# Performance work log

Measured on AMD Instinct MI355X. Metric: run time of the kernel, lower is better.

## Reference

```python
import jax, jax.numpy as jnp
import numpy as np

N_NODES = 50000
N_EDGES = 600000
D_IN = 128
D_HID = 128


def setup_inputs() -> dict:
    key = jax.random.key(0)
    ks = jax.random.split(key, 12)
    edge_index = jax.random.randint(ks[0], (2, N_EDGES), 0, N_NODES)
    x = jax.random.normal(ks[1], (N_NODES, D_IN), dtype=jnp.float32)
    shuffled_x = jax.random.normal(ks[2], (N_NODES, D_IN), dtype=jnp.float32)
    # DIMPLayer params: linear transform applied after neighbor aggregation
    sc = 1.0 / np.sqrt(D_IN)
    W0 = jax.random.uniform(ks[3], (D_IN, D_HID), jnp.float32, -sc, sc)
    b0 = jnp.zeros((D_HID,), jnp.float32)
    W1 = jax.random.uniform(ks[4], (D_HID, D_HID), jnp.float32, -sc, sc)
    b1 = jnp.zeros((D_HID,), jnp.float32)
    W2 = jax.random.uniform(ks[5], (D_HID, D_HID), jnp.float32, -sc, sc)
    b2 = jnp.zeros((D_HID,), jnp.float32)
    # Bilinear discriminator weight
    Wd = jax.random.uniform(ks[6], (D_HID, D_HID), jnp.float32, -sc, sc)
    return {"edge_index": edge_index, "x": x, "shuffled_x": shuffled_x,
            "W0": W0, "b0": b0, "W1": W1, "b1": b1, "W2": W2, "b2": b2,
            "Wd": Wd}


def reference(edge_index, x, shuffled_x, W0, b0, W1, b1, W2, b2, Wd):
    src, dst = edge_index[0], edge_index[1]
    n = x.shape[0]

    def dimp_layer(h, W, b):
        # gather source-node features along edges, scatter-add into destinations
        agg = jax.ops.segment_sum(h[src], dst, num_segments=n)  # [N, d]
        return jax.nn.relu(agg @ W + b)

    params = [(W0, b0), (W1, b1), (W2, b2)]

    def encode(feat):
        h = feat
        for W, b in params:
            h = dimp_layer(h, W, b)
        return h

    h = encode(x)                    # [N, D_HID]
    s = jnp.mean(h, axis=0)          # [D_HID] graph summary
    shuffled_h = encode(shuffled_x)  # [N, D_HID]

    # Bilinear discriminator: logit_i = h_i^T Wd s
    ws = Wd @ s                      # [D_HID]
    d_h = h @ ws                     # [N]
    d_shuffled_h = shuffled_h @ ws   # [N]
    return jnp.concatenate((d_h, d_shuffled_h), axis=0)  # [2N]
```

## Files before the change

kernel.cpp:

```cpp
#include <hip/hip_runtime.h>

#define D 128

typedef short bf16x8 __attribute__((ext_vector_type(8)));
typedef float f32x4 __attribute__((ext_vector_type(4)));

static __device__ __forceinline__ unsigned short f2bf(float f) {
    unsigned int u = __float_as_uint(f);
    u = u + 0x7FFFu + ((u >> 16) & 1u);
    return (unsigned short)(u >> 16);
}
static __device__ __forceinline__ float bf2f(unsigned short h) {
    return __uint_as_float(((unsigned int)h) << 16);
}


__global__ __launch_bounds__(256) void count_kernel(const int* __restrict__ dst,
        int* __restrict__ counts, int E) {
    int e = blockIdx.x * 256 + threadIdx.x;
    if (e < E) atomicAdd(&counts[dst[e]], 1);
}

__global__ __launch_bounds__(256) void scan_reduce(const int* __restrict__ counts,
        int* __restrict__ bsum, int n) {
    int b = blockIdx.x, t = threadIdx.x;
    int base = b * 1024 + t * 4;
    int s = 0;
    #pragma unroll
    for (int i = 0; i < 4; ++i) {
        int idx = base + i;
        if (idx < n) s += counts[idx];
    }
    __shared__ int sd[256];
    sd[t] = s;
    __syncthreads();
    #pragma unroll
    for (int off = 128; off > 0; off >>= 1) {
        if (t < off) sd[t] += sd[t + off];
        __syncthreads();
    }
    if (t == 0) bsum[b] = sd[0];
}

__global__ __launch_bounds__(64) void scan_tops(const int* __restrict__ bsum,
        int* __restrict__ bofs, int* __restrict__ row_ptr_end, int B) {
    int t = threadIdx.x;
    int v = (t < B) ? bsum[t] : 0;
    int inc = v;
    #pragma unroll
    for (int off = 1; off < 64; off <<= 1) {
        int u = __shfl_up(inc, off);
        if (t >= off) inc += u;
    }
    if (t < B) bofs[t] = inc - v;
    if (t == 63) *row_ptr_end = inc;
}

__global__ __launch_bounds__(256) void scan_final(const int* __restrict__ counts,
        const int* __restrict__ bofs, int* __restrict__ row_ptr,
        int* __restrict__ cursor, int n) {
    int b = blockIdx.x, t = threadIdx.x;
    int base = b * 1024 + t * 4;
    int v[4];
    int s = 0;
    #pragma unroll
    for (int i = 0; i < 4; ++i) {
        int idx = base + i;
        v[i] = (idx < n) ? counts[idx] : 0;
        s += v[i];
    }
    __shared__ int sd[256];
    sd[t] = s;
    __syncthreads();
    #pragma unroll
    for (int off = 1; off < 256; off <<= 1) {
        int u = (t >= off) ? sd[t - off] : 0;
        __syncthreads();
        sd[t] += u;
        __syncthreads();
    }
    int excl = bofs[b] + sd[t] - s;
    #pragma unroll
    for (int i = 0; i < 4; ++i) {
        int idx = base + i;
        if (idx < n) {
            row_ptr[idx] = excl;
            cursor[idx] = excl;
            excl += v[i];
        }
    }
}

__global__ __launch_bounds__(256) void fill_kernel(const int* __restrict__ src,
        const int* __restrict__ dst, int* __restrict__ cursor,
        int* __restrict__ src_sorted, int E) {
    int e = blockIdx.x * 256 + threadIdx.x;
    if (e < E) {
        int p = atomicAdd(&cursor[dst[e]], 1);
        src_sorted[p] = src[e];
    }
}


__global__ __launch_bounds__(256) void cvt_kernel(const float* __restrict__ in,
        unsigned short* __restrict__ out, int n4) {
    int i = blockIdx.x * 256 + threadIdx.x;
    if (i < n4) {
        float4 v = ((const float4*)in)[i];
        ushort4 o;
        o.x = f2bf(v.x); o.y = f2bf(v.y); o.z = f2bf(v.z); o.w = f2bf(v.w);
        ((ushort4*)out)[i] = o;
    }
}


__global__ __launch_bounds__(256) void pack_w(const float* __restrict__ W,
        unsigned short* __restrict__ Wp) {
    int t = blockIdx.x * 256 + threadIdx.x;
    if (t >= 2048) return;
    int lane = t & 63;
    int ct = (t >> 6) & 7;
    int s = t >> 9;
    int n = ct * 16 + (lane & 15);
    int k0 = s * 32 + (lane >> 4) * 8;
    unsigned short hi[8], lo[8];
    #pragma unroll
    for (int j = 0; j < 8; ++j) {
        float f = W[(size_t)(k0 + j) * 128 + n];
        unsigned short h = f2bf(f);
        hi[j] = h;
        lo[j] = f2bf(f - bf2f(h));
    }
    size_t bh = ((size_t)((s * 8 + ct) * 2 + 0) * 64 + lane) * 8;
    size_t bl = ((size_t)((s * 8 + ct) * 2 + 1) * 64 + lane) * 8;
    #pragma unroll
    for (int j = 0; j < 8; ++j) { Wp[bh + j] = hi[j]; Wp[bl + j] = lo[j]; }
}


__global__ __launch_bounds__(512, 8) void agg_gemm(const unsigned short* __restrict__ Hin,
        const int* __restrict__ row_ptr, const int* __restrict__ src_sorted,
        const unsigned short* __restrict__ Wp, const float* __restrict__ bias,
        unsigned short* __restrict__ Hout, int N, int NT,
        float* __restrict__ mean_out, int Nmean, float inv_n) {
    __shared__ float Af[64][129];
    __shared__ float red[8][64];
    int tid = threadIdx.x;
    int bm = blockIdx.x * 64;

    {
        int lane = tid & 15;
        int ng   = tid >> 4;
        const uint4* h4 = (const uint4*)Hin;

        auto addv = [](float* a, uint4 v) {
            a[0] += __uint_as_float(v.x << 16);
            a[1] += __uint_as_float(v.x & 0xFFFF0000u);
            a[2] += __uint_as_float(v.y << 16);
            a[3] += __uint_as_float(v.y & 0xFFFF0000u);
            a[4] += __uint_as_float(v.z << 16);
            a[5] += __uint_as_float(v.z & 0xFFFF0000u);
            a[6] += __uint_as_float(v.w << 16);
            a[7] += __uint_as_float(v.w & 0xFFFF0000u);
        };

        #pragma unroll
        for (int g = 0; g < 2; ++g) {
            int local = g * 32 + ng;
            int node = bm + local; if (node >= NT) node = NT - 1;
            int base = (node < N) ? 0 : N;
            int rp = node - base;
            int beg = row_ptr[rp], end = row_ptr[rp + 1];

            float acc[8];
            #pragma unroll
            for (int i = 0; i < 8; ++i) acc[i] = 0.f;

            int j = beg;
            for (; j + 3 < end; j += 4) {
                uint4 v0 = h4[(size_t)(src_sorted[j    ] + base) * 16 + lane];
                uint4 v1 = h4[(size_t)(src_sorted[j + 1] + base) * 16 + lane];
                uint4 v2 = h4[(size_t)(src_sorted[j + 2] + base) * 16 + lane];
                uint4 v3 = h4[(size_t)(src_sorted[j + 3] + base) * 16 + lane];
                addv(acc, v0); addv(acc, v1); addv(acc, v2); addv(acc, v3);
            }
            for (; j < end; ++j) {
                uint4 v0 = h4[(size_t)(src_sorted[j] + base) * 16 + lane];
                addv(acc, v0);
            }
            #pragma unroll
            for (int i = 0; i < 8; ++i) Af[local][lane * 8 + i] = acc[i];
        }
    }
    __syncthreads();

    int w = tid >> 6, l = tid & 63;
    int fr = l & 15;
    int kg = l >> 4;
    int rt = w & 3;
    int ch = w >> 2;
    int m0 = bm + rt * 16;

    f32x4 acc[4];
    #pragma unroll
    for (int cl = 0; cl < 4; ++cl) acc[cl] = (f32x4){0.f, 0.f, 0.f, 0.f};

    const float* arow = &Af[rt * 16 + fr][0];
    const uint4* wp4 = (const uint4*)Wp;

    for (int s = 0; s < 4; ++s) {
        bf16x8 a_hi, a_lo;
        #pragma unroll
        for (int jj = 0; jj < 8; ++jj) {
            float f = arow[s * 32 + kg * 8 + jj];
            unsigned short h = f2bf(f);
            a_hi[jj] = (short)h;
            a_lo[jj] = (short)f2bf(f - bf2f(h));
        }
        #pragma unroll
        for (int cl = 0; cl < 4; ++cl) {
            int ct = ch * 4 + cl;
            uint4 bhu = wp4[(size_t)((s * 8 + ct) * 2 + 0) * 64 + l];
            uint4 blu = wp4[(size_t)((s * 8 + ct) * 2 + 1) * 64 + l];
            bf16x8 b_hi, b_lo;
            *(uint4*)&b_hi = bhu;
            *(uint4*)&b_lo = blu;
            acc[cl] = __builtin_amdgcn_mfma_f32_16x16x32_bf16(a_hi, b_hi, acc[cl], 0, 0, 0);
            acc[cl] = __builtin_amdgcn_mfma_f32_16x16x32_bf16(a_lo, b_hi, acc[cl], 0, 0, 0);
            acc[cl] = __builtin_amdgcn_mfma_f32_16x16x32_bf16(a_hi, b_lo, acc[cl], 0, 0, 0);
        }
    }

    float colsum[4];
    #pragma unroll
    for (int cl = 0; cl < 4; ++cl) {
        int col = (ch * 4 + cl) * 16 + fr;
        float b = bias[col];
        float cs = 0.f;
        #pragma unroll
        for (int r = 0; r < 4; ++r) {
            int m = m0 + kg * 4 + r;
            float v = fmaxf(acc[cl][r] + b, 0.f);
            if (m < NT) Hout[(size_t)m * 128 + col] = f2bf(v);
            if (m < Nmean) cs += v;
        }
        colsum[cl] = cs;
    }

    if (mean_out) {
        #pragma unroll
        for (int cl = 0; cl < 4; ++cl) {
            float v = colsum[cl];
            v += __shfl_xor(v, 16);
            v += __shfl_xor(v, 32);
            if (l < 16) red[w][cl * 16 + l] = v;
        }
        __syncthreads();
        if (tid < 128) {
            int half = tid >> 6;
            int cl = tid & 63;
            float s = red[half * 4 + 0][cl] + red[half * 4 + 1][cl]
                    + red[half * 4 + 2][cl] + red[half * 4 + 3][cl];
            if (s != 0.f) atomicAdd(&mean_out[tid], s * inv_n);
        }
    }
}


__global__ __launch_bounds__(128) void wd_kernel(const float* __restrict__ Wd,
        const float* __restrict__ s, float* __restrict__ wsv) {
    __shared__ float sl[128];
    int i = threadIdx.x;
    sl[i] = s[i];
    __syncthreads();
    float acc = 0.f;
    for (int j = 0; j < 128; ++j) acc += Wd[(size_t)i * 128 + j] * sl[j];
    wsv[i] = acc;
}


__global__ __launch_bounds__(256) void disc_kernel(const unsigned short* __restrict__ h,
        const float* __restrict__ wsv, float* __restrict__ out, int n) {
    int wave = threadIdx.x >> 6, lane = threadIdx.x & 63;
    int node = blockIdx.x * 4 + wave;
    if (node >= n) return;
    unsigned int hv = ((const unsigned int*)h)[(size_t)node * 64 + lane];
    float2 wv = *(const float2*)&wsv[lane * 2];
    float lo = __uint_as_float(hv << 16);
    float hi = __uint_as_float(hv & 0xFFFF0000u);
    float acc = lo * wv.x + hi * wv.y;
    #pragma unroll
    for (int off = 32; off > 0; off >>= 1) acc += __shfl_down(acc, off);
    if (lane == 0) out[node] = acc;
}


extern "C" void kernel_launch(void* const* d_in, const int* in_sizes, int n_in,
                              void* d_out, int out_size, void* d_ws, size_t ws_size,
                              hipStream_t stream) {
    const int* edge_index = (const int*)d_in[0];
    const float* x  = (const float*)d_in[1];
    const float* sx = (const float*)d_in[2];
    const float* W0 = (const float*)d_in[3];
    const float* b0 = (const float*)d_in[4];
    const float* W1 = (const float*)d_in[5];
    const float* b1 = (const float*)d_in[6];
    const float* W2 = (const float*)d_in[7];
    const float* b2 = (const float*)d_in[8];
    const float* Wd = (const float*)d_in[9];
    float* out = (float*)d_out;

    const int E = in_sizes[0] / 2;
    const int N = in_sizes[1] / D;
    const int* src = edge_index;
    const int* dst = edge_index + E;
    const float inv_n = 1.0f / (float)N;

    char* wsp = (char*)d_ws;
    size_t off = 0;
    auto alloc = [&](size_t bytes) -> void* {
        void* p = wsp + off;
        off += (bytes + 511) & ~(size_t)511;
        return p;
    };
    int* counts     = (int*)alloc((size_t)N * 4);
    int* row_ptr    = (int*)alloc((size_t)(N + 1) * 4);
    int* cursor     = (int*)alloc((size_t)N * 4);
    int* src_sorted = (int*)alloc((size_t)E * 4);
    int* bsum       = (int*)alloc(64 * 4);
    int* bofs       = (int*)alloc(64 * 4);
    float* svec     = (float*)alloc(D * 4);
    float* wsv      = (float*)alloc(D * 4);
    unsigned short* wp0 = (unsigned short*)alloc((size_t)D * D * 2 * 2);
    unsigned short* wp1 = (unsigned short*)alloc((size_t)D * D * 2 * 2);
    unsigned short* wp2 = (unsigned short*)alloc((size_t)D * D * 2 * 2);

    size_t fixed = off;
    size_t need_batched = fixed + 2 * ((size_t)2 * N * D * 2 + 512);
    bool batched = ws_size >= need_batched;
    int NB = batched ? 2 * N : N;

    unsigned short* hbufA = (unsigned short*)alloc((size_t)NB * D * 2);
    unsigned short* hbufB = (unsigned short*)alloc((size_t)NB * D * 2);

    hipMemsetAsync(counts, 0, (size_t)N * 4, stream);
    hipMemsetAsync(svec, 0, D * 4, stream);

    pack_w<<<8, 256, 0, stream>>>(W0, wp0);
    pack_w<<<8, 256, 0, stream>>>(W1, wp1);
    pack_w<<<8, 256, 0, stream>>>(W2, wp2);

    int eblocks = (E + 255) / 256;
    int sblocks = (N + 1023) / 1024;
    count_kernel<<<eblocks, 256, 0, stream>>>(dst, counts, E);
    scan_reduce<<<sblocks, 256, 0, stream>>>(counts, bsum, N);
    scan_tops<<<1, 64, 0, stream>>>(bsum, bofs, row_ptr + N, sblocks);
    scan_final<<<sblocks, 256, 0, stream>>>(counts, bofs, row_ptr, cursor, N);
    fill_kernel<<<eblocks, 256, 0, stream>>>(src, dst, cursor, src_sorted, E);

    int n4 = N * D / 4;
    int cblocks = (n4 + 255) / 256;
    int gblocks = (NB + 63) / 64;

    if (batched) {
        cvt_kernel<<<cblocks, 256, 0, stream>>>(x, hbufA, n4);
        cvt_kernel<<<cblocks, 256, 0, stream>>>(sx, hbufA + (size_t)N * D, n4);
        agg_gemm<<<gblocks, 512, 0, stream>>>(hbufA, row_ptr, src_sorted, wp0, b0,
                                              hbufB, N, NB, nullptr, 0, 0.f);
        agg_gemm<<<gblocks, 512, 0, stream>>>(hbufB, row_ptr, src_sorted, wp1, b1,
                                              hbufA, N, NB, nullptr, 0, 0.f);
        agg_gemm<<<gblocks, 512, 0, stream>>>(hbufA, row_ptr, src_sorted, wp2, b2,
                                              hbufB, N, NB, svec, N, inv_n);
        wd_kernel<<<1, 128, 0, stream>>>(Wd, svec, wsv);
        disc_kernel<<<(NB + 3) / 4, 256, 0, stream>>>(hbufB, wsv, out, NB);
    } else {
        auto encode = [&](const float* input, float* mean_out) {
            cvt_kernel<<<cblocks, 256, 0, stream>>>(input, hbufA, n4);
            agg_gemm<<<gblocks, 512, 0, stream>>>(hbufA, row_ptr, src_sorted, wp0, b0,
                                                  hbufB, N, NB, nullptr, 0, 0.f);
            agg_gemm<<<gblocks, 512, 0, stream>>>(hbufB, row_ptr, src_sorted, wp1, b1,
                                                  hbufA, N, NB, nullptr, 0, 0.f);
            agg_gemm<<<gblocks, 512, 0, stream>>>(hbufA, row_ptr, src_sorted, wp2, b2,
                                                  hbufB, N, NB, mean_out, mean_out ? N : 0, inv_n);
        };
        encode(x, svec);
        wd_kernel<<<1, 128, 0, stream>>>(Wd, svec, wsv);
        disc_kernel<<<(NB + 3) / 4, 256, 0, stream>>>(hbufB, wsv, out, NB);
        encode(sx, nullptr);
        disc_kernel<<<(NB + 3) / 4, 256, 0, stream>>>(hbufB, wsv, out + N, NB);
    }
}
```

Measured before the change: 299.3 us.

## Pair real and shuffled node rows in one block to share edge index traversal

In batched mode each block now handles 32 node indices for both the real and the shuffled encoder. It walks each CSR row once and gathers both feature rows per edge, filling the two 32-row halves of the shared tile. This halves the reads of row_ptr and src_sorted and doubles the independent loads in flight per edge. The output indexing is remapped to match. In exchange, each thread holds more accumulator registers, and the unroll drops from 4 to 2 edges.

```diff
diff --git a/kernel.cpp b/kernel.cpp
--- a/kernel.cpp
+++ b/kernel.cpp
@@ -141,12 +141,13 @@
 __global__ __launch_bounds__(512, 8) void agg_gemm(const unsigned short* __restrict__ Hin,
         const int* __restrict__ row_ptr, const int* __restrict__ src_sorted,
         const unsigned short* __restrict__ Wp, const float* __restrict__ bias,
-        unsigned short* __restrict__ Hout, int N, int NT,
+        unsigned short* __restrict__ Hout, int N, int NT, int paired,
         float* __restrict__ mean_out, int Nmean, float inv_n) {
     __shared__ float Af[64][129];
     __shared__ float red[8][64];
     int tid = threadIdx.x;
     int bm = blockIdx.x * 64;
+    int pb = blockIdx.x * 32;
 
     {
         int lane = tid & 15;
@@ -164,32 +165,65 @@
             a[7] += __uint_as_float(v.w & 0xFFFF0000u);
         };
 
-        #pragma unroll
-        for (int g = 0; g < 2; ++g) {
-            int local = g * 32 + ng;
-            int node = bm + local; if (node >= NT) node = NT - 1;
-            int base = (node < N) ? 0 : N;
-            int rp = node - base;
-            int beg = row_ptr[rp], end = row_ptr[rp + 1];
-
-            float acc[8];
+        if (paired) {
+            int p = pb + ng; if (p >= N) p = N - 1;
+            int beg = row_ptr[p], end = row_ptr[p + 1];
+            size_t mofs = (size_t)N * 16;
+
+            float accA[8], accB[8];
             #pragma unroll
-            for (int i = 0; i < 8; ++i) acc[i] = 0.f;
+            for (int i = 0; i < 8; ++i) { accA[i] = 0.f; accB[i] = 0.f; }
 
             int j = beg;
-            for (; j + 3 < end; j += 4) {
-                uint4 v0 = h4[(size_t)(src_sorted[j    ] + base) * 16 + lane];
-                uint4 v1 = h4[(size_t)(src_sorted[j + 1] + base) * 16 + lane];
-                uint4 v2 = h4[(size_t)(src_sorted[j + 2] + base) * 16 + lane];
-                uint4 v3 = h4[(size_t)(src_sorted[j + 3] + base) * 16 + lane];
-                addv(acc, v0); addv(acc, v1); addv(acc, v2); addv(acc, v3);
-            }
-            for (; j < end; ++j) {
-                uint4 v0 = h4[(size_t)(src_sorted[j] + base) * 16 + lane];
-                addv(acc, v0);
+            for (; j + 1 < end; j += 2) {
+                size_t r0 = (size_t)src_sorted[j]     * 16 + lane;
+                size_t r1 = (size_t)src_sorted[j + 1] * 16 + lane;
+                uint4 a0 = h4[r0];
+                uint4 b0 = h4[r0 + mofs];
+                uint4 a1 = h4[r1];
+                uint4 b1 = h4[r1 + mofs];
+                addv(accA, a0); addv(accB, b0);
+                addv(accA, a1); addv(accB, b1);
+            }
+            if (j < end) {
+                size_t r0 = (size_t)src_sorted[j] * 16 + lane;
+                uint4 a0 = h4[r0];
+                uint4 b0 = h4[r0 + mofs];
+                addv(accA, a0); addv(accB, b0);
             }
             #pragma unroll
-            for (int i = 0; i < 8; ++i) Af[local][lane * 8 + i] = acc[i];
+            for (int i = 0; i < 8; ++i) {
+                Af[ng][lane * 8 + i]      = accA[i];
+                Af[32 + ng][lane * 8 + i] = accB[i];
+            }
+        } else {
+            #pragma unroll
+            for (int g = 0; g < 2; ++g) {
+                int local = g * 32 + ng;
+                int node = bm + local; if (node >= NT) node = NT - 1;
+                int base = (node < N) ? 0 : N;
+                int rp = node - base;
+                int beg = row_ptr[rp], end = row_ptr[rp + 1];
+
+                float acc[8];
+                #pragma unroll
+                for (int i = 0; i < 8; ++i) acc[i] = 0.f;
+
+                int j = beg;
+                for (; j + 3 < end; j += 4) {
+                    uint4 v0 = h4[(size_t)(src_sorted[j    ] + base) * 16 + lane];
+                    uint4 v1 = h4[(size_t)(src_sorted[j + 1] + base) * 16 + lane];
+                    uint4 v2 = h4[(size_t)(src_sorted[j + 2] + base) * 16 + lane];
+                    uint4 v3 = h4[(size_t)(src_sorted[j + 3] + base) * 16 + lane];
+                    addv(acc, v0); addv(acc, v1); addv(acc, v2); addv(acc, v3);
+                }
+                for (; j < end; ++j) {
+                    uint4 v0 = h4[(size_t)(src_sorted[j] + base) * 16 + lane];
+                    addv(acc, v0);
+                }
+                #pragma unroll
+                for (int i = 0; i < 8; ++i) Af[local][lane * 8 + i] = acc[i];
+            }
         }
     }
     __syncthreads();
@@ -199,7 +233,6 @@
     int kg = l >> 4;
     int rt = w & 3;
     int ch = w >> 2;
-    int m0 = bm + rt * 16;
 
     f32x4 acc[4];
     #pragma unroll
@@ -239,10 +272,21 @@
         float cs = 0.f;
         #pragma unroll
         for (int r = 0; r < 4; ++r) {
-            int m = m0 + kg * 4 + r;
+            int lm = rt * 16 + kg * 4 + r;
             float v = fmaxf(acc[cl][r] + b, 0.f);
-            if (m < NT) Hout[(size_t)m * 128 + col] = f2bf(v);
-            if (m < Nmean) cs += v;
+            int node; bool valid;
+            if (paired) {
+                int pr = (lm < 32) ? lm : (lm - 32);
+                valid = (pb + pr) < N;
+                node = pb + pr + ((lm < 32) ? 0 : N);
+            } else {
+                node = bm + lm;
+                valid = node < NT;
+            }
+            if (valid) {
+                Hout[(size_t)node * 128 + col] = f2bf(v);
+                if (node < Nmean) cs += v;
+            }
         }
         colsum[cl] = cs;
     }
@@ -339,6 +383,7 @@
     size_t need_batched = fixed + 2 * ((size_t)2 * N * D * 2 + 512);
     bool batched = ws_size >= need_batched;
     int NB = batched ? 2 * N : N;
+    int paired = batched ? 1 : 0;
 
     unsigned short* hbufA = (unsigned short*)alloc((size_t)NB * D * 2);
     unsigned short* hbufB = (unsigned short*)alloc((size_t)NB * D * 2);
@@ -360,28 +405,28 @@
 
     int n4 = N * D / 4;
     int cblocks = (n4 + 255) / 256;
-    int gblocks = (NB + 63) / 64;
+    int gblocks = paired ? (N + 31) / 32 : (NB + 63) / 64;
 
     if (batched) {
         cvt_kernel<<<cblocks, 256, 0, stream>>>(x, hbufA, n4);
         cvt_kernel<<<cblocks, 256, 0, stream>>>(sx, hbufA + (size_t)N * D, n4);
         agg_gemm<<<gblocks, 512, 0, stream>>>(hbufA, row_ptr, src_sorted, wp0, b0,
-                                              hbufB, N, NB, nullptr, 0, 0.f);
+                                              hbufB, N, NB, paired, nullptr, 0, 0.f);
         agg_gemm<<<gblocks, 512, 0, stream>>>(hbufB, row_ptr, src_sorted, wp1, b1,
-                                              hbufA, N, NB, nullptr, 0, 0.f);
+                                              hbufA, N, NB, paired, nullptr, 0, 0.f);
         agg_gemm<<<gblocks, 512, 0, stream>>>(hbufA, row_ptr, src_sorted, wp2, b2,
-                                              hbufB, N, NB, svec, N, inv_n);
+                                              hbufB, N, NB, paired, svec, N, inv_n);
         wd_kernel<<<1, 128, 0, stream>>>(Wd, svec, wsv);
         disc_kernel<<<(NB + 3) / 4, 256, 0, stream>>>(hbufB, wsv, out, NB);
     } else {
         auto encode = [&](const float* input, float* mean_out) {
             cvt_kernel<<<cblocks, 256, 0, stream>>>(input, hbufA, n4);
             agg_gemm<<<gblocks, 512, 0, stream>>>(hbufA, row_ptr, src_sorted, wp0, b0,
-                                                  hbufB, N, NB, nullptr, 0, 0.f);
+                                                  hbufB, N, NB, paired, nullptr, 0, 0.f);
             agg_gemm<<<gblocks, 512, 0, stream>>>(hbufB, row_ptr, src_sorted, wp1, b1,
-                                                  hbufA, N, NB, nullptr, 0, 0.f);
+                                                  hbufA, N, NB, paired, nullptr, 0, 0.f);
             agg_gemm<<<gblocks, 512, 0, stream>>>(hbufA, row_ptr, src_sorted, wp2, b2,
-                                                  hbufB, N, NB, mean_out, mean_out ? N : 0, inv_n);
+                                                  hbufB, N, NB, paired, mean_out, mean_out ? N : 0, inv_n);
         };
         encode(x, svec);
         wd_kernel<<<1, 128, 0, stream>>>(Wd, svec, wsv);
```

Measured after the change: 319.3 us. +6.7%, slower.
